# Optimization experiments

Measured on AMD Instinct MI355X. Metric: run time of the kernel, lower is better.

## Reference

```python
import jax, jax.numpy as jnp
import numpy as np

_CLIP = 1e4

def _n2n(t):
    return jnp.nan_to_num(t, nan=0.0, posinf=_CLIP, neginf=-_CLIP)

def setup_inputs() -> dict:
    key = jax.random.key(0)
    ks = jax.random.split(key, 9)
    B, N, E, DH, DM = 4, 16384, 65536, 128, 64
    s = 0.05
    return {
        "x": jax.random.normal(ks[0], (B, N, 3), jnp.float32),
        "h": jax.random.normal(ks[1], (B, N, DH), jnp.float32),
        "edge_index": jax.random.randint(ks[2], (B, E, 2), 0, N, jnp.int64 if jax.config.jax_enable_x64 else jnp.int32),
        "pe_w1": jax.random.normal(ks[3], (2 * DH + 1, DM), jnp.float32) * s,
        "pe_b1": jnp.zeros((DM,), jnp.float32),
        "pe_w2": jax.random.normal(ks[4], (DM, DM), jnp.float32) * s,
        "pe_b2": jnp.zeros((DM,), jnp.float32),
        "px_w": jax.random.normal(ks[5], (DM, 1), jnp.float32) * s,
        "ph_w1": jax.random.normal(ks[6], (DH + DM, DH), jnp.float32) * s,
        "ph_b1": jnp.zeros((DH,), jnp.float32),
        "ph_w2": jax.random.normal(ks[7], (DH, DH), jnp.float32) * s,
        "ph_b2": jnp.zeros((DH,), jnp.float32),
    }

def reference(x, h, edge_index, pe_w1, pe_b1, pe_w2, pe_b2, px_w, ph_w1, ph_b1, ph_w2, ph_b2):
    B = x.shape[0]
    src = edge_index[:, :, 0]          # [B,E]
    dst = edge_index[:, :, 1]
    bidx = jnp.arange(B)[:, None]      # [B,1] for batched gather/scatter
    x_i = x[bidx, src]                 # [B,E,3]
    x_j = x[bidx, dst]
    h_i = h[bidx, src]                 # [B,E,DH]
    h_j = h[bidx, dst]
    diff = x_i - x_j
    dist2 = jnp.clip((diff ** 2).sum(-1, keepdims=True), 1e-12, None)  # [B,E,1]
    edge_input = _n2n(jnp.concatenate([h_i, h_j, dist2], axis=-1))
    # phi_e: Linear -> SiLU -> Linear -> SiLU
    m = jax.nn.silu(edge_input @ pe_w1 + pe_b1)
    m_ij = _n2n(jax.nn.silu(m @ pe_w2 + pe_b2))   # [B,E,DM]
    m_x = m_ij @ px_w                             # [B,E,1]
    direction = diff / (jnp.sqrt(dist2) + 1e-8)
    delta_x_ij = _n2n(m_x * direction)            # [B,E,3]
    delta_x = jnp.zeros_like(x).at[bidx, src].add(delta_x_ij)
    delta_h_msg = jnp.zeros((B, x.shape[1], m_ij.shape[-1]), h.dtype).at[bidx, src].add(m_ij)
    h_input = jnp.concatenate([h, delta_h_msg], axis=-1)
    h_new = h + jax.nn.silu(h_input @ ph_w1 + ph_b1) @ ph_w2 + ph_b2
    x_new = x + delta_x
    return _n2n(x_new), _n2n(h_new)
```

## Files before the change

kernel.cpp:

```cpp
#include <hip/hip_runtime.h>


typedef unsigned short ushort_t;
typedef __attribute__((ext_vector_type(8))) short bf16x8;
typedef __attribute__((ext_vector_type(4))) float f32x4;
typedef _Float16 h2 __attribute__((ext_vector_type(2)));

__device__ __forceinline__ float fast_rcp(float v) { return __builtin_amdgcn_rcpf(v); }
__device__ __forceinline__ float fast_silu(float v) { return v * fast_rcp(1.0f + __expf(-v)); }
__device__ __forceinline__ ushort_t f2bf(float f) {
    unsigned u = __float_as_uint(f);
    u += 0x7fffu + ((u >> 16) & 1u);
    return (ushort_t)(u >> 16);
}
__device__ __forceinline__ float bf2f(ushort_t b) {
    return __uint_as_float(((unsigned)b) << 16);
}
__device__ __forceinline__ h2 u2h2(unsigned u) {
    union { unsigned u; h2 h; } v; v.u = u; return v.h;
}

__global__ __launch_bounds__(256) void init_k(const float* __restrict__ pe_w1,
                                              const float* __restrict__ pe_w2,
                                              const float* __restrict__ ph_w1,
                                              const float* __restrict__ ph_w2,
                                              int* __restrict__ cursor,
                                              ushort_t* __restrict__ W1t,
                                              ushort_t* __restrict__ Wp1t,
                                              ushort_t* __restrict__ Wp2t,
                                              unsigned* __restrict__ w2h) {
    int gg = blockIdx.x * 256 + threadIdx.x;
    if (gg < 65536) { cursor[gg] = 0; return; }
    int g = gg - 65536;
    if (g < 16384) {
        int c = g >> 7, k = g & 127;
        float v = (c < 64) ? pe_w1[k * 64 + c] : pe_w1[(128 + k) * 64 + (c - 64)];
        W1t[g] = f2bf(v);
    } else if (g < 40960) {
        int g2 = g - 16384;
        int n = g2 / 192, k = g2 - n * 192;
        Wp1t[g2] = f2bf(ph_w1[k * 128 + n]);
    } else if (g < 57344) {
        int g3 = g - 40960;
        int n = g3 >> 7, k = g3 & 127;
        Wp2t[g3] = f2bf(ph_w2[k * 128 + n]);
    } else if (g < 59392) {
        int g4 = g - 57344;
        int k2 = g4 >> 6, c = g4 & 63;
        union { unsigned u; _Float16 h[2]; } p;
        p.h[0] = (_Float16)pe_w2[(2 * k2) * 64 + c];
        p.h[1] = (_Float16)pe_w2[(2 * k2 + 1) * 64 + c];
        w2h[g4] = p.u;
    }
}

__global__ __launch_bounds__(256) void scatter_k(const int* __restrict__ ei,
                                                 int* __restrict__ cursor,
                                                 int* __restrict__ elist) {
    int e = blockIdx.x * 256 + threadIdx.x;
    int2 sd = ((const int2*)ei)[e];
    int b = e >> 16;
    int gi = (b << 14) + sd.x;
    int gj = (b << 14) + sd.y;
    int slot = atomicAdd(&cursor[gi], 1);
    if (slot < 64) elist[gi * 64 + slot] = gj;
}

__global__ __launch_bounds__(64, 4) void node_k(const float* __restrict__ x,
                                                const ushort_t* __restrict__ P,
                                                const int* __restrict__ cursor,
                                                const int* __restrict__ elist,
                                                const float* __restrict__ w1,
                                                const float* __restrict__ b1,
                                                const unsigned* __restrict__ w2h,
                                                const float* __restrict__ b2,
                                                const float* __restrict__ pxw,
                                                ushort_t* __restrict__ dh,
                                                float* __restrict__ outx) {
    const int n = blockIdx.x;
    const int lane = threadIdx.x;
    __shared__ unsigned m_u[32];
    ushort_t* mh = (ushort_t*)m_u;

    const float w1r = w1[256 * 64 + lane];
    const float b1v = b1[lane];
    const float b2v = b2[lane];
    const float pxv = pxw[lane];
    const float Pi = bf2f(P[(size_t)n * 128 + lane]);
    const float xi0 = x[n * 3 + 0];
    const float xi1 = x[n * 3 + 1];
    const float xi2 = x[n * 3 + 2];

    float dhacc = 0.0f;
    float dxp0 = 0.0f, dxp1 = 0.0f, dxp2 = 0.0f;
    const int dg = min(cursor[n], 64);
    const int base = n * 64;

    for (int t = 0; t < dg; t++) {
        int gj = elist[base + t];
        float Pj = bf2f(P[(size_t)gj * 128 + 64 + lane]);
        float ddx = xi0 - x[gj * 3 + 0];
        float ddy = xi1 - x[gj * 3 + 1];
        float ddz = xi2 - x[gj * 3 + 2];
        float d2 = fmaxf(ddx * ddx + ddy * ddy + ddz * ddz, 1e-12f);
        float m = fast_silu(Pi + Pj + d2 * w1r + b1v);
        __builtin_amdgcn_wave_barrier();
        union { ushort_t s; _Float16 h; } mc;
        mc.h = (_Float16)m;
        mh[lane] = mc.s;
        __builtin_amdgcn_wave_barrier();
        float s = b2v;
#pragma unroll
        for (int k2 = 0; k2 < 32; k2++) {
            h2 mm = u2h2(m_u[k2]);
            h2 ww = u2h2(w2h[k2 * 64 + lane]);
            s = __builtin_amdgcn_fdot2(mm, ww, s, false);
        }
        __builtin_amdgcn_wave_barrier();
        float m2 = fast_silu(s);
        dhacc += m2;
        float c = m2 * pxv * fast_rcp(sqrtf(d2) + 1e-8f);
        dxp0 = fmaf(c, ddx, dxp0);
        dxp1 = fmaf(c, ddy, dxp1);
        dxp2 = fmaf(c, ddz, dxp2);
    }

    dh[(size_t)n * 64 + lane] = f2bf(dhacc);

    for (int off = 32; off; off >>= 1) {
        dxp0 += __shfl_down(dxp0, off);
        dxp1 += __shfl_down(dxp1, off);
        dxp2 += __shfl_down(dxp2, off);
    }
    if (lane == 0) {
        outx[n * 3 + 0] = xi0 + dxp0;
        outx[n * 3 + 1] = xi1 + dxp1;
        outx[n * 3 + 2] = xi2 + dxp2;
    }
}

template <bool EMIT_BF16>
__global__ __launch_bounds__(256, 2) void pgemm_k(const float* __restrict__ A0,
                                                  const ushort_t* __restrict__ Wt,
                                                  ushort_t* __restrict__ outP,
                                                  ushort_t* __restrict__ hbout) {
    constexpr int KPAD = 40;
    __shared__ ushort_t As[128 * KPAD];
    __shared__ ushort_t Bs[128 * KPAD];
    const int tid = threadIdx.x;
    const int m0 = blockIdx.x * 128;
    const int wave = tid >> 6;
    const int lane = tid & 63;
    const int lr = lane & 15;
    const int lq = lane >> 4;

    f32x4 acc[2][8];
#pragma unroll
    for (int mt = 0; mt < 2; mt++)
#pragma unroll
        for (int nt = 0; nt < 8; nt++) { f32x4 z = {0.f,0.f,0.f,0.f}; acc[mt][nt] = z; }

    for (int k0 = 0; k0 < 128; k0 += 32) {
#pragma unroll
        for (int i = 0; i < 4; i++) {
            int lin = tid + i * 256;
            int m = lin >> 3;
            int kq = (lin & 7) * 4;
            float4 v = *(const float4*)(A0 + (size_t)(m0 + m) * 128 + k0 + kq);
            ushort4 w4;
            w4.x = f2bf(v.x); w4.y = f2bf(v.y); w4.z = f2bf(v.z); w4.w = f2bf(v.w);
            if (EMIT_BF16)
                *(ushort4*)(hbout + (size_t)(m0 + m) * 128 + k0 + kq) = w4;
            *(ushort4*)&As[m * KPAD + kq] = w4;
        }
#pragma unroll
        for (int i = 0; i < 2; i++) {
            int lin = tid + i * 256;
            int n = lin >> 2;
            int kq = (lin & 3) * 8;
            *(uint4*)&Bs[n * KPAD + kq] = *(const uint4*)(Wt + (size_t)n * 128 + k0 + kq);
        }
        __syncthreads();
        bf16x8 af[2], bfr[8];
#pragma unroll
        for (int mt = 0; mt < 2; mt++)
            af[mt] = *(const bf16x8*)&As[(wave * 32 + mt * 16 + lr) * KPAD + lq * 8];
#pragma unroll
        for (int nt = 0; nt < 8; nt++)
            bfr[nt] = *(const bf16x8*)&Bs[(nt * 16 + lr) * KPAD + lq * 8];
#pragma unroll
        for (int mt = 0; mt < 2; mt++)
#pragma unroll
            for (int nt = 0; nt < 8; nt++)
                acc[mt][nt] = __builtin_amdgcn_mfma_f32_16x16x32_bf16(af[mt], bfr[nt], acc[mt][nt], 0, 0, 0);
        __syncthreads();
    }
#pragma unroll
    for (int mt = 0; mt < 2; mt++)
#pragma unroll
        for (int nt = 0; nt < 8; nt++)
#pragma unroll
            for (int r = 0; r < 4; r++) {
                int row = m0 + wave * 32 + mt * 16 + lq * 4 + r;
                int col = nt * 16 + lr;
                outP[(size_t)row * 128 + col] = f2bf(acc[mt][nt][r]);
            }
}

template <bool USE_HB>
__global__ __launch_bounds__(256, 2) void mlp_fused_k(const float* __restrict__ h,
                                                      const ushort_t* __restrict__ hb,
                                                      const ushort_t* __restrict__ dh,
                                                      const ushort_t* __restrict__ Wp1t,
                                                      const float* __restrict__ b1,
                                                      const ushort_t* __restrict__ Wp2t,
                                                      const float* __restrict__ b2,
                                                      float* __restrict__ outh) {
    constexpr int KPAD = 40, TPAD = 136;
    __shared__ ushort_t As[128 * KPAD];
    __shared__ ushort_t Bs[128 * KPAD];
    __shared__ ushort_t Ts[128 * TPAD];
    const int tid = threadIdx.x;
    const int m0 = blockIdx.x * 128;
    const int wave = tid >> 6;
    const int lane = tid & 63;
    const int lr = lane & 15;
    const int lq = lane >> 4;

    f32x4 acc[2][8];
#pragma unroll
    for (int mt = 0; mt < 2; mt++)
#pragma unroll
        for (int nt = 0; nt < 8; nt++) { f32x4 z = {0.f,0.f,0.f,0.f}; acc[mt][nt] = z; }

    for (int k0 = 0; k0 < 192; k0 += 32) {
        if (USE_HB) {
#pragma unroll
            for (int i = 0; i < 2; i++) {
                int lin = tid + i * 256;
                int m = lin >> 2;
                int kq = (lin & 3) * 8;
                const ushort_t* src = (k0 >= 128)
                    ? dh + (size_t)(m0 + m) * 64 + (k0 - 128 + kq)
                    : hb + (size_t)(m0 + m) * 128 + k0 + kq;
                *(uint4*)&As[m * KPAD + kq] = *(const uint4*)src;
            }
        } else {
#pragma unroll
            for (int i = 0; i < 4; i++) {
                int lin = tid + i * 256;
                int m = lin >> 3;
                int kq = (lin & 7) * 4;
                ushort4 w4;
                if (k0 >= 128) {
                    w4 = *(const ushort4*)(dh + (size_t)(m0 + m) * 64 + (k0 - 128 + kq));
                } else {
                    float4 v = *(const float4*)(h + (size_t)(m0 + m) * 128 + k0 + kq);
                    w4.x = f2bf(v.x); w4.y = f2bf(v.y); w4.z = f2bf(v.z); w4.w = f2bf(v.w);
                }
                *(ushort4*)&As[m * KPAD + kq] = w4;
            }
        }
#pragma unroll
        for (int i = 0; i < 2; i++) {
            int lin = tid + i * 256;
            int n = lin >> 2;
            int kq = (lin & 3) * 8;
            *(uint4*)&Bs[n * KPAD + kq] = *(const uint4*)(Wp1t + (size_t)n * 192 + k0 + kq);
        }
        __syncthreads();
        bf16x8 af[2], bfr[8];
#pragma unroll
        for (int mt = 0; mt < 2; mt++)
            af[mt] = *(const bf16x8*)&As[(wave * 32 + mt * 16 + lr) * KPAD + lq * 8];
#pragma unroll
        for (int nt = 0; nt < 8; nt++)
            bfr[nt] = *(const bf16x8*)&Bs[(nt * 16 + lr) * KPAD + lq * 8];
#pragma unroll
        for (int mt = 0; mt < 2; mt++)
#pragma unroll
            for (int nt = 0; nt < 8; nt++)
                acc[mt][nt] = __builtin_amdgcn_mfma_f32_16x16x32_bf16(af[mt], bfr[nt], acc[mt][nt], 0, 0, 0);
        __syncthreads();
    }
#pragma unroll
    for (int mt = 0; mt < 2; mt++)
#pragma unroll
        for (int nt = 0; nt < 8; nt++)
#pragma unroll
            for (int r = 0; r < 4; r++) {
                int row = wave * 32 + mt * 16 + lq * 4 + r;
                int col = nt * 16 + lr;
                Ts[row * TPAD + col] = f2bf(fast_silu(acc[mt][nt][r] + b1[col]));
            }
    __syncthreads();

    f32x4 acc2[2][8];
#pragma unroll
    for (int mt = 0; mt < 2; mt++)
#pragma unroll
        for (int nt = 0; nt < 8; nt++) { f32x4 z = {0.f,0.f,0.f,0.f}; acc2[mt][nt] = z; }

    for (int k0 = 0; k0 < 128; k0 += 32) {
#pragma unroll
        for (int i = 0; i < 2; i++) {
            int lin = tid + i * 256;
            int n = lin >> 2;
            int kq = (lin & 3) * 8;
            *(uint4*)&Bs[n * KPAD + kq] = *(const uint4*)(Wp2t + (size_t)n * 128 + k0 + kq);
        }
        __syncthreads();
        bf16x8 af[2], bfr[8];
#pragma unroll
        for (int mt = 0; mt < 2; mt++)
            af[mt] = *(const bf16x8*)&Ts[(wave * 32 + mt * 16 + lr) * TPAD + k0 + lq * 8];
#pragma unroll
        for (int nt = 0; nt < 8; nt++)
            bfr[nt] = *(const bf16x8*)&Bs[(nt * 16 + lr) * KPAD + lq * 8];
#pragma unroll
        for (int mt = 0; mt < 2; mt++)
#pragma unroll
            for (int nt = 0; nt < 8; nt++)
                acc2[mt][nt] = __builtin_amdgcn_mfma_f32_16x16x32_bf16(af[mt], bfr[nt], acc2[mt][nt], 0, 0, 0);
        __syncthreads();
    }
#pragma unroll
    for (int mt = 0; mt < 2; mt++)
#pragma unroll
        for (int nt = 0; nt < 8; nt++)
#pragma unroll
            for (int r = 0; r < 4; r++) {
                int row = m0 + wave * 32 + mt * 16 + lq * 4 + r;
                int col = nt * 16 + lr;
                float v = acc2[mt][nt][r] + b2[col];
                if (USE_HB) v += bf2f(hb[(size_t)row * 128 + col]);
                else        v += h[(size_t)row * 128 + col];
                outh[(size_t)row * 128 + col] = v;
            }
}

extern "C" void kernel_launch(void* const* d_in, const int* in_sizes, int n_in,
                              void* d_out, int out_size, void* d_ws, size_t ws_size,
                              hipStream_t stream) {
    const float* x     = (const float*)d_in[0];
    const float* h     = (const float*)d_in[1];
    const int*   ei    = (const int*)d_in[2];
    const float* pe_w1 = (const float*)d_in[3];
    const float* pe_b1 = (const float*)d_in[4];
    const float* pe_w2 = (const float*)d_in[5];
    const float* pe_b2 = (const float*)d_in[6];
    const float* px_w  = (const float*)d_in[7];
    const float* ph_w1 = (const float*)d_in[8];
    const float* ph_b1 = (const float*)d_in[9];
    const float* ph_w2 = (const float*)d_in[10];
    const float* ph_b2 = (const float*)d_in[11];

    float* outx = (float*)d_out;
    float* outh = (float*)d_out + 196608;

    ushort_t* P    = (ushort_t*)d_ws;
    ushort_t* dh   = P + (size_t)65536 * 128;
    int* cursor    = (int*)(dh + (size_t)65536 * 64);
    int* elist     = cursor + 65536;
    ushort_t* W1t  = (ushort_t*)(elist + (size_t)65536 * 64);
    ushort_t* Wp1t = W1t + 16384;
    ushort_t* Wp2t = Wp1t + 24576;
    unsigned* w2h  = (unsigned*)(Wp2t + 16384);
    ushort_t* hb   = (ushort_t*)(w2h + 4096);
    size_t need_hb = (size_t)((char*)(hb + (size_t)65536 * 128) - (char*)d_ws);
    const bool use_hb = ws_size >= need_hb;

    init_k<<<488, 256, 0, stream>>>(pe_w1, pe_w2, ph_w1, ph_w2,
                                    cursor, W1t, Wp1t, Wp2t, w2h);
    if (use_hb)
        pgemm_k<true><<<512, 256, 0, stream>>>(h, W1t, P, hb);
    else
        pgemm_k<false><<<512, 256, 0, stream>>>(h, W1t, P, nullptr);
    scatter_k<<<1024, 256, 0, stream>>>(ei, cursor, elist);
    node_k<<<65536, 64, 0, stream>>>(x, P, cursor, elist,
                                     pe_w1, pe_b1, w2h, pe_b2, px_w,
                                     dh, outx);
    if (use_hb)
        mlp_fused_k<true><<<512, 256, 0, stream>>>(h, hb, dh, Wp1t, ph_b1,
                                                   Wp2t, ph_b2, outh);
    else
        mlp_fused_k<false><<<512, 256, 0, stream>>>(h, nullptr, dh, Wp1t, ph_b1,
                                                    Wp2t, ph_b2, outh);
}
```

Before: 196.3 us.

## Pack four nodes per block and process edges in pairs in node kernel

The node kernel now runs four wavefronts per 256-thread block, one node each, instead of one 64-thread block per node. Each wavefront loads its neighbour list once into lanes and broadcasts indices with readlane instead of re-reading memory per edge. Edges are processed two at a time, sharing the W2 weight loads across both, with 128-bit LDS reads and four independent dot-product accumulators. The b1 bias is folded into the per-node constant. The aim is less launch and scheduling overhead, more instruction-level parallelism and fewer weight loads, at the cost of higher register pressure and a changed summation order.

```diff
diff --git a/kernel.cpp b/kernel.cpp
--- a/kernel.cpp
+++ b/kernel.cpp
@@ -66,27 +66,28 @@
     if (slot < 64) elist[gi * 64 + slot] = gj;
 }
 
-__global__ __launch_bounds__(64, 4) void node_k(const float* __restrict__ x,
-                                                const ushort_t* __restrict__ P,
-                                                const int* __restrict__ cursor,
-                                                const int* __restrict__ elist,
-                                                const float* __restrict__ w1,
-                                                const float* __restrict__ b1,
-                                                const unsigned* __restrict__ w2h,
-                                                const float* __restrict__ b2,
-                                                const float* __restrict__ pxw,
-                                                ushort_t* __restrict__ dh,
-                                                float* __restrict__ outx) {
-    const int n = blockIdx.x;
-    const int lane = threadIdx.x;
-    __shared__ unsigned m_u[32];
-    ushort_t* mh = (ushort_t*)m_u;
+__global__ __launch_bounds__(256, 8) void node_k(const float* __restrict__ x,
+                                                 const ushort_t* __restrict__ P,
+                                                 const int* __restrict__ cursor,
+                                                 const int* __restrict__ elist,
+                                                 const float* __restrict__ w1,
+                                                 const float* __restrict__ b1,
+                                                 const unsigned* __restrict__ w2h,
+                                                 const float* __restrict__ b2,
+                                                 const float* __restrict__ pxw,
+                                                 ushort_t* __restrict__ dh,
+                                                 float* __restrict__ outx) {
+    const int wid = threadIdx.x >> 6;
+    const int lane = threadIdx.x & 63;
+    const int n = blockIdx.x * 4 + wid;
+    __shared__ __attribute__((aligned(16))) unsigned m_u[4][2][32];
+    ushort_t* mh0 = (ushort_t*)m_u[wid][0];
+    ushort_t* mh1 = (ushort_t*)m_u[wid][1];
 
     const float w1r = w1[256 * 64 + lane];
-    const float b1v = b1[lane];
     const float b2v = b2[lane];
     const float pxv = pxw[lane];
-    const float Pi = bf2f(P[(size_t)n * 128 + lane]);
+    const float Pib = bf2f(P[(size_t)n * 128 + lane]) + b1[lane];
     const float xi0 = x[n * 3 + 0];
     const float xi1 = x[n * 3 + 1];
     const float xi2 = x[n * 3 + 2];
@@ -96,33 +97,90 @@
     const int dg = min(cursor[n], 64);
     const int base = n * 64;
 
-    for (int t = 0; t < dg; t++) {
-        int gj = elist[base + t];
+    int gjv = 0;
+    if (lane < dg) gjv = elist[base + lane];
+
+    int t = 0;
+    for (; t + 2 <= dg; t += 2) {
+        const int gjA = __builtin_amdgcn_readlane(gjv, t);
+        const int gjB = __builtin_amdgcn_readlane(gjv, t + 1);
+        float PjA = bf2f(P[(size_t)gjA * 128 + 64 + lane]);
+        float PjB = bf2f(P[(size_t)gjB * 128 + 64 + lane]);
+        float ax = xi0 - x[gjA * 3 + 0];
+        float ay = xi1 - x[gjA * 3 + 1];
+        float az = xi2 - x[gjA * 3 + 2];
+        float bx = xi0 - x[gjB * 3 + 0];
+        float by = xi1 - x[gjB * 3 + 1];
+        float bz = xi2 - x[gjB * 3 + 2];
+        float d2A = fmaxf(ax * ax + ay * ay + az * az, 1e-12f);
+        float d2B = fmaxf(bx * bx + by * by + bz * bz, 1e-12f);
+        float mA = fast_silu(Pib + PjA + d2A * w1r);
+        float mB = fast_silu(Pib + PjB + d2B * w1r);
+        union { ushort_t s; _Float16 h; } ca, cb;
+        ca.h = (_Float16)mA;
+        cb.h = (_Float16)mB;
+        __builtin_amdgcn_wave_barrier();
+        mh0[lane] = ca.s;
+        mh1[lane] = cb.s;
+        __builtin_amdgcn_wave_barrier();
+        float a0 = b2v, a1 = 0.f, a2 = 0.f, a3 = 0.f;
+        float e0 = b2v, e1 = 0.f, e2 = 0.f, e3 = 0.f;
+#pragma unroll
+        for (int q = 0; q < 8; q++) {
+            uint4 mmA = *(const uint4*)&m_u[wid][0][q * 4];
+            uint4 mmB = *(const uint4*)&m_u[wid][1][q * 4];
+            h2 w0 = u2h2(w2h[(4 * q + 0) * 64 + lane]);
+            h2 w1q = u2h2(w2h[(4 * q + 1) * 64 + lane]);
+            h2 w2q = u2h2(w2h[(4 * q + 2) * 64 + lane]);
+            h2 w3 = u2h2(w2h[(4 * q + 3) * 64 + lane]);
+            a0 = __builtin_amdgcn_fdot2(u2h2(mmA.x), w0, a0, false);
+            e0 = __builtin_amdgcn_fdot2(u2h2(mmB.x), w0, e0, false);
+            a1 = __builtin_amdgcn_fdot2(u2h2(mmA.y), w1q, a1, false);
+            e1 = __builtin_amdgcn_fdot2(u2h2(mmB.y), w1q, e1, false);
+            a2 = __builtin_amdgcn_fdot2(u2h2(mmA.z), w2q, a2, false);
+            e2 = __builtin_amdgcn_fdot2(u2h2(mmB.z), w2q, e2, false);
+            a3 = __builtin_amdgcn_fdot2(u2h2(mmA.w), w3, a3, false);
+            e3 = __builtin_amdgcn_fdot2(u2h2(mmB.w), w3, e3, false);
+        }
+        __builtin_amdgcn_wave_barrier();
+        float m2A = fast_silu((a0 + a1) + (a2 + a3));
+        float m2B = fast_silu((e0 + e1) + (e2 + e3));
+        dhacc += m2A + m2B;
+        float cA = m2A * pxv * fast_rcp(sqrtf(d2A) + 1e-8f);
+        float cB = m2B * pxv * fast_rcp(sqrtf(d2B) + 1e-8f);
+        dxp0 = fmaf(cA, ax, fmaf(cB, bx, dxp0));
+        dxp1 = fmaf(cA, ay, fmaf(cB, by, dxp1));
+        dxp2 = fmaf(cA, az, fmaf(cB, bz, dxp2));
+    }
+    if (t < dg) {
+        const int gj = __builtin_amdgcn_readlane(gjv, t);
         float Pj = bf2f(P[(size_t)gj * 128 + 64 + lane]);
-        float ddx = xi0 - x[gj * 3 + 0];
-        float ddy = xi1 - x[gj * 3 + 1];
-        float ddz = xi2 - x[gj * 3 + 2];
-        float d2 = fmaxf(ddx * ddx + ddy * ddy + ddz * ddz, 1e-12f);
-        float m = fast_silu(Pi + Pj + d2 * w1r + b1v);
-        __builtin_amdgcn_wave_barrier();
+        float ax = xi0 - x[gj * 3 + 0];
+        float ay = xi1 - x[gj * 3 + 1];
+        float az = xi2 - x[gj * 3 + 2];
+        float d2 = fmaxf(ax * ax + ay * ay + az * az, 1e-12f);
+        float m = fast_silu(Pib + Pj + d2 * w1r);
         union { ushort_t s; _Float16 h; } mc;
         mc.h = (_Float16)m;
-        mh[lane] = mc.s;
-        __builtin_amdgcn_wave_barrier();
-        float s = b2v;
-#pragma unroll
-        for (int k2 = 0; k2 < 32; k2++) {
-            h2 mm = u2h2(m_u[k2]);
-            h2 ww = u2h2(w2h[k2 * 64 + lane]);
-            s = __builtin_amdgcn_fdot2(mm, ww, s, false);
-        }
-        __builtin_amdgcn_wave_barrier();
-        float m2 = fast_silu(s);
+        __builtin_amdgcn_wave_barrier();
+        mh0[lane] = mc.s;
+        __builtin_amdgcn_wave_barrier();
+        float a0 = b2v, a1 = 0.f, a2 = 0.f, a3 = 0.f;
+#pragma unroll
+        for (int q = 0; q < 8; q++) {
+            uint4 mm = *(const uint4*)&m_u[wid][0][q * 4];
+            a0 = __builtin_amdgcn_fdot2(u2h2(mm.x), u2h2(w2h[(4 * q + 0) * 64 + lane]), a0, false);
+            a1 = __builtin_amdgcn_fdot2(u2h2(mm.y), u2h2(w2h[(4 * q + 1) * 64 + lane]), a1, false);
+            a2 = __builtin_amdgcn_fdot2(u2h2(mm.z), u2h2(w2h[(4 * q + 2) * 64 + lane]), a2, false);
+            a3 = __builtin_amdgcn_fdot2(u2h2(mm.w), u2h2(w2h[(4 * q + 3) * 64 + lane]), a3, false);
+        }
+        __builtin_amdgcn_wave_barrier();
+        float m2 = fast_silu((a0 + a1) + (a2 + a3));
         dhacc += m2;
         float c = m2 * pxv * fast_rcp(sqrtf(d2) + 1e-8f);
-        dxp0 = fmaf(c, ddx, dxp0);
-        dxp1 = fmaf(c, ddy, dxp1);
-        dxp2 = fmaf(c, ddz, dxp2);
+        dxp0 = fmaf(c, ax, dxp0);
+        dxp1 = fmaf(c, ay, dxp1);
+        dxp2 = fmaf(c, az, dxp2);
     }
 
     dh[(size_t)n * 64 + lane] = f2bf(dhacc);
@@ -377,9 +435,9 @@
     else
         pgemm_k<false><<<512, 256, 0, stream>>>(h, W1t, P, nullptr);
     scatter_k<<<1024, 256, 0, stream>>>(ei, cursor, elist);
-    node_k<<<65536, 64, 0, stream>>>(x, P, cursor, elist,
-                                     pe_w1, pe_b1, w2h, pe_b2, px_w,
-                                     dh, outx);
+    node_k<<<16384, 256, 0, stream>>>(x, P, cursor, elist,
+                                      pe_w1, pe_b1, w2h, pe_b2, px_w,
+                                      dh, outx);
     if (use_hb)
         mlp_fused_k<true><<<512, 256, 0, stream>>>(h, hb, dh, Wp1t, ph_b1,
                                                    Wp2t, ph_b2, outh);
```

New measurement: 293.5 us. 49.5% more time.

## Process four edges per wave in node kernel with 4-wide lane channel tiling

Applied to the files above, without the earlier changes.

Restructures the per-node edge loop so each 64-lane wave handles four edges at once, with 16 lanes per edge and four output channels per lane. Edge indices are loaded once into a register and broadcast with shuffles, and the second-layer fp16 dot products read the weights as vectorized uint4 loads. The px projection is reduced across 16 lanes with xor shuffles, and the dh accumulators are reduced across the four groups at the end. This cuts loop trip count and serial latency per node, at the cost of more shuffles and masked work on the last partial group of edges.

```diff
diff --git a/kernel.cpp b/kernel.cpp
--- a/kernel.cpp
+++ b/kernel.cpp
@@ -5,6 +5,7 @@
 typedef __attribute__((ext_vector_type(8))) short bf16x8;
 typedef __attribute__((ext_vector_type(4))) float f32x4;
 typedef _Float16 h2 __attribute__((ext_vector_type(2)));
+typedef __fp16 fp16x2 __attribute__((ext_vector_type(2)));
 
 __device__ __forceinline__ float fast_rcp(float v) { return __builtin_amdgcn_rcpf(v); }
 __device__ __forceinline__ float fast_silu(float v) { return v * fast_rcp(1.0f + __expf(-v)); }
@@ -16,8 +17,15 @@
 __device__ __forceinline__ float bf2f(ushort_t b) {
     return __uint_as_float(((unsigned)b) << 16);
 }
+__device__ __forceinline__ float bflo(unsigned u) { return __uint_as_float(u << 16); }
+__device__ __forceinline__ float bfhi(unsigned u) { return __uint_as_float(u & 0xffff0000u); }
 __device__ __forceinline__ h2 u2h2(unsigned u) {
     union { unsigned u; h2 h; } v; v.u = u; return v.h;
+}
+__device__ __forceinline__ unsigned pk2u(float a, float b) {
+    union { fp16x2 h; unsigned u; } v;
+    v.h = __builtin_amdgcn_cvt_pkrtz(a, b);
+    return v.u;
 }
 
 __global__ __launch_bounds__(256) void init_k(const float* __restrict__ pe_w1,
@@ -79,53 +87,109 @@
                                                 float* __restrict__ outx) {
     const int n = blockIdx.x;
     const int lane = threadIdx.x;
-    __shared__ unsigned m_u[32];
-    ushort_t* mh = (ushort_t*)m_u;
-
-    const float w1r = w1[256 * 64 + lane];
-    const float b1v = b1[lane];
-    const float b2v = b2[lane];
-    const float pxv = pxw[lane];
-    const float Pi = bf2f(P[(size_t)n * 128 + lane]);
+    const int q = lane & 15;
+    const int g = lane >> 4;
+    __shared__ __attribute__((aligned(16))) unsigned mlds[4][32];
+
+    const float4 w1r4 = *(const float4*)(w1 + 256 * 64 + q * 4);
+    const float4 b1v4 = *(const float4*)(b1 + q * 4);
+    const float4 b2v4 = *(const float4*)(b2 + q * 4);
+    float4 px4 = *(const float4*)(pxw + q * 4);
+    px4.x *= 0.0625f; px4.y *= 0.0625f; px4.z *= 0.0625f; px4.w *= 0.0625f;
+
+    uint2 piu = *(const uint2*)(P + (size_t)n * 128 + q * 4);
+    const float pib0 = bflo(piu.x) + b1v4.x;
+    const float pib1 = bfhi(piu.x) + b1v4.y;
+    const float pib2 = bflo(piu.y) + b1v4.z;
+    const float pib3 = bfhi(piu.y) + b1v4.w;
+
     const float xi0 = x[n * 3 + 0];
     const float xi1 = x[n * 3 + 1];
     const float xi2 = x[n * 3 + 2];
 
-    float dhacc = 0.0f;
-    float dxp0 = 0.0f, dxp1 = 0.0f, dxp2 = 0.0f;
     const int dg = min(cursor[n], 64);
-    const int base = n * 64;
-
-    for (int t = 0; t < dg; t++) {
-        int gj = elist[base + t];
-        float Pj = bf2f(P[(size_t)gj * 128 + 64 + lane]);
-        float ddx = xi0 - x[gj * 3 + 0];
-        float ddy = xi1 - x[gj * 3 + 1];
-        float ddz = xi2 - x[gj * 3 + 2];
+    int gjv = 0;
+    if (lane < dg) gjv = elist[n * 64 + lane];
+
+    float dh0 = 0.f, dh1 = 0.f, dh2 = 0.f, dh3 = 0.f;
+    float dxp0 = 0.f, dxp1 = 0.f, dxp2 = 0.f;
+
+    const int nt = (dg + 3) >> 2;
+    for (int t = 0; t < nt; t++) {
+        const int slot = t * 4 + g;
+        const int gj = __shfl(gjv, slot);
+        const float act = (slot < dg) ? 1.0f : 0.0f;
+
+        uint2 pj = *(const uint2*)(P + (size_t)gj * 128 + 64 + q * 4);
+        float xj0 = x[gj * 3 + 0];
+        float xj1 = x[gj * 3 + 1];
+        float xj2 = x[gj * 3 + 2];
+        float ddx = xi0 - xj0, ddy = xi1 - xj1, ddz = xi2 - xj2;
         float d2 = fmaxf(ddx * ddx + ddy * ddy + ddz * ddz, 1e-12f);
-        float m = fast_silu(Pi + Pj + d2 * w1r + b1v);
+        float m0 = fast_silu(fmaf(d2, w1r4.x, pib0 + bflo(pj.x)));
+        float m1 = fast_silu(fmaf(d2, w1r4.y, pib1 + bfhi(pj.x)));
+        float m2v = fast_silu(fmaf(d2, w1r4.z, pib2 + bflo(pj.y)));
+        float m3 = fast_silu(fmaf(d2, w1r4.w, pib3 + bfhi(pj.y)));
+        uint2 mp;
+        mp.x = pk2u(m0, m1);
+        mp.y = pk2u(m2v, m3);
         __builtin_amdgcn_wave_barrier();
-        union { ushort_t s; _Float16 h; } mc;
-        mc.h = (_Float16)m;
-        mh[lane] = mc.s;
+        *(uint2*)&mlds[g][2 * q] = mp;
         __builtin_amdgcn_wave_barrier();
-        float s = b2v;
-#pragma unroll
-        for (int k2 = 0; k2 < 32; k2++) {
-            h2 mm = u2h2(m_u[k2]);
-            h2 ww = u2h2(w2h[k2 * 64 + lane]);
-            s = __builtin_amdgcn_fdot2(mm, ww, s, false);
+
+        float s0 = b2v4.x, s1 = b2v4.y, s2 = b2v4.z, s3 = b2v4.w;
+#pragma unroll
+        for (int k8 = 0; k8 < 8; k8++) {
+            uint4 mm = *(const uint4*)&mlds[g][k8 * 4];
+            uint4 wa = *(const uint4*)(w2h + (4 * k8 + 0) * 64 + q * 4);
+            uint4 wb = *(const uint4*)(w2h + (4 * k8 + 1) * 64 + q * 4);
+            uint4 wc = *(const uint4*)(w2h + (4 * k8 + 2) * 64 + q * 4);
+            uint4 wd = *(const uint4*)(w2h + (4 * k8 + 3) * 64 + q * 4);
+            s0 = __builtin_amdgcn_fdot2(u2h2(mm.x), u2h2(wa.x), s0, false);
+            s1 = __builtin_amdgcn_fdot2(u2h2(mm.x), u2h2(wa.y), s1, false);
+            s2 = __builtin_amdgcn_fdot2(u2h2(mm.x), u2h2(wa.z), s2, false);
+            s3 = __builtin_amdgcn_fdot2(u2h2(mm.x), u2h2(wa.w), s3, false);
+            s0 = __builtin_amdgcn_fdot2(u2h2(mm.y), u2h2(wb.x), s0, false);
+            s1 = __builtin_amdgcn_fdot2(u2h2(mm.y), u2h2(wb.y), s1, false);
+            s2 = __builtin_amdgcn_fdot2(u2h2(mm.y), u2h2(wb.z), s2, false);
+            s3 = __builtin_amdgcn_fdot2(u2h2(mm.y), u2h2(wb.w), s3, false);
+            s0 = __builtin_amdgcn_fdot2(u2h2(mm.z), u2h2(wc.x), s0, false);
+            s1 = __builtin_amdgcn_fdot2(u2h2(mm.z), u2h2(wc.y), s1, false);
+            s2 = __builtin_amdgcn_fdot2(u2h2(mm.z), u2h2(wc.z), s2, false);
+            s3 = __builtin_amdgcn_fdot2(u2h2(mm.z), u2h2(wc.w), s3, false);
+            s0 = __builtin_amdgcn_fdot2(u2h2(mm.w), u2h2(wd.x), s0, false);
+            s1 = __builtin_amdgcn_fdot2(u2h2(mm.w), u2h2(wd.y), s1, false);
+            s2 = __builtin_amdgcn_fdot2(u2h2(mm.w), u2h2(wd.z), s2, false);
+            s3 = __builtin_amdgcn_fdot2(u2h2(mm.w), u2h2(wd.w), s3, false);
         }
         __builtin_amdgcn_wave_barrier();
-        float m2 = fast_silu(s);
-        dhacc += m2;
-        float c = m2 * pxv * fast_rcp(sqrtf(d2) + 1e-8f);
-        dxp0 = fmaf(c, ddx, dxp0);
-        dxp1 = fmaf(c, ddy, dxp1);
-        dxp2 = fmaf(c, ddz, dxp2);
-    }
-
-    dh[(size_t)n * 64 + lane] = f2bf(dhacc);
+
+        float o0 = fast_silu(s0) * act;
+        float o1 = fast_silu(s1) * act;
+        float o2 = fast_silu(s2) * act;
+        float o3 = fast_silu(s3) * act;
+        dh0 += o0; dh1 += o1; dh2 += o2; dh3 += o3;
+        float mxp = o0 * px4.x + o1 * px4.y + o2 * px4.z + o3 * px4.w;
+        mxp += __shfl_xor(mxp, 1);
+        mxp += __shfl_xor(mxp, 2);
+        mxp += __shfl_xor(mxp, 4);
+        mxp += __shfl_xor(mxp, 8);
+        float cmul = mxp * fast_rcp(sqrtf(d2) + 1e-8f);
+        dxp0 = fmaf(cmul, ddx, dxp0);
+        dxp1 = fmaf(cmul, ddy, dxp1);
+        dxp2 = fmaf(cmul, ddz, dxp2);
+    }
+
+    dh0 += __shfl_xor(dh0, 16); dh0 += __shfl_xor(dh0, 32);
+    dh1 += __shfl_xor(dh1, 16); dh1 += __shfl_xor(dh1, 32);
+    dh2 += __shfl_xor(dh2, 16); dh2 += __shfl_xor(dh2, 32);
+    dh3 += __shfl_xor(dh3, 16); dh3 += __shfl_xor(dh3, 32);
+    if (g == 0) {
+        uint2 dpack;
+        dpack.x = (unsigned)f2bf(dh0) | ((unsigned)f2bf(dh1) << 16);
+        dpack.y = (unsigned)f2bf(dh2) | ((unsigned)f2bf(dh3) << 16);
+        *(uint2*)(dh + (size_t)n * 64 + q * 4) = dpack;
+    }
 
     for (int off = 32; off; off >>= 1) {
         dxp0 += __shfl_down(dxp0, off);
@@ -183,7 +247,7 @@
         __syncthreads();
         bf16x8 af[2], bfr[8];
 #pragma unroll
-        for (int mt = 0; mt < 2; mt++)
+    for (int mt = 0; mt < 2; mt++)
             af[mt] = *(const bf16x8*)&As[(wave * 32 + mt * 16 + lr) * KPAD + lq * 8];
 #pragma unroll
         for (int nt = 0; nt < 8; nt++)
```

New measurement: 520.9 us. 165% more time.
